# Kernel tuning notes

Measured on AMD Instinct MI355X. Metric: run time of the kernel, lower is better.

Reference implementation:

```python
import jax, jax.numpy as jnp
import numpy as np

N = 50000
E = 400000
IN_DIM = 16
EMB = 32
HID = 128
HEADS = 4
LAYERS = 3
EPS_BN = 1e-5
NEG_SLOPE = 0.2


def setup_inputs() -> dict:
    key = jax.random.key(0)
    ks = jax.random.split(key, 16)
    s = 0.1
    C = HID  # per-head out channels (concat=False)
    inp = {
        "x": jax.random.normal(ks[0], (N, IN_DIM), jnp.float32),
        "edge_index": jax.random.randint(ks[1], (2, E), 0, N, jnp.int64),
        "emb": s * jax.random.normal(ks[2], (N, EMB), jnp.float32),
        "Wf": s * jax.random.normal(ks[3], (EMB, IN_DIM), jnp.float32),
        "bf": jnp.zeros((EMB,), jnp.float32),
        "Wc": s * jax.random.normal(ks[4], (HID, 2 * EMB), jnp.float32),
        "bc": jnp.zeros((HID,), jnp.float32),
        "Wl": s * jax.random.normal(ks[5], (LAYERS, HEADS * C, HID), jnp.float32),
        "a_src": s * jax.random.normal(ks[6], (LAYERS, HEADS, C), jnp.float32),
        "a_dst": s * jax.random.normal(ks[7], (LAYERS, HEADS, C), jnp.float32),
        "bl": jnp.zeros((LAYERS, C), jnp.float32),
        "gamma": jnp.ones((LAYERS, C), jnp.float32),
        "beta": jnp.zeros((LAYERS, C), jnp.float32),
        "Wout": s * jax.random.normal(ks[8], (1, HID), jnp.float32),
        "bout": jnp.zeros((1,), jnp.float32),
    }
    return inp


def _gat_layer(h, src, dst, W, a_s, a_d, b):
    n = h.shape[0]
    C = W.shape[0] // HEADS
    hp = (h @ W.T).reshape(n, HEADS, C)                # (N,H,C)
    al_s = jnp.sum(hp * a_s, axis=-1)                  # (N,H)
    al_d = jnp.sum(hp * a_d, axis=-1)                  # (N,H)
    e = jax.nn.leaky_relu(al_s[src] + al_d[dst], NEG_SLOPE)  # (E,H)
    m = jax.ops.segment_max(e, dst, num_segments=n)    # per-target max
    ex = jnp.exp(e - m[dst])
    denom = jax.ops.segment_sum(ex, dst, num_segments=n) + 1e-16
    alpha = ex / denom[dst]                            # (E,H)
    msg = hp[src] * alpha[..., None]                   # (E,H,C)
    out = jax.ops.segment_sum(msg, dst, num_segments=n)
    return jnp.mean(out, axis=1) + b                   # concat=False: head mean


def _bn(x, g, b):
    mu = jnp.mean(x, axis=0)
    var = jnp.var(x, axis=0)  # biased, as torch BN uses for normalization
    return (x - mu) * jax.lax.rsqrt(var + EPS_BN) * g + b


def reference(x, edge_index, emb, Wf, bf, Wc, bc, Wl, a_src, a_dst, bl, gamma, beta, Wout, bout):
    n = x.shape[0]
    loop = jnp.arange(n, dtype=edge_index.dtype)
    src = jnp.concatenate([edge_index[0], loop])       # add self loops
    dst = jnp.concatenate([edge_index[1], loop])
    feat = x @ Wf.T + bf
    h = jax.nn.relu(jnp.concatenate([emb, feat], axis=1) @ Wc.T + bc)
    prev_h = h
    for i in range(LAYERS):
        h = _gat_layer(h, src, dst, Wl[i], a_src[i], a_dst[i], bl[i])
        h = jax.nn.relu(_bn(h, gamma[i], beta[i]))
        if prev_h.shape == h.shape:
            h = h + prev_h
        prev_h = h
    out = h @ Wout.T + bout
    return jnp.clip(out, -10.0, 10.0)
```

## Files before the change

kernel.cpp:

```cpp
#include <hip/hip_runtime.h>
#include <hip/hip_bf16.h>
#include <math.h>

#define INDIM 16
#define EMBD 32
#define UDIM 64
#define HIDD 128
#define HEADS 4
#define LAYERS 3
#define MPAD 50048

typedef short v8s __attribute__((ext_vector_type(8)));
typedef float v4f __attribute__((ext_vector_type(4)));

__device__ __forceinline__ float lrelu(float x) { return x > 0.f ? x : 0.2f * x; }
__device__ __forceinline__ float bf2f(unsigned int bits16) {
    unsigned int u = bits16 << 16;
    return __builtin_bit_cast(float, u);
}
__device__ __forceinline__ unsigned short f2bf(float f) {
    unsigned int u = __builtin_bit_cast(unsigned int, f);
    unsigned int lsb = (u >> 16) & 1;
    u += 0x7fff + lsb;
    return (unsigned short)(u >> 16);
}

__global__ __launch_bounds__(256) void k_enc(const float* __restrict__ x,
                                             const float* __restrict__ emb,
                                             const float* __restrict__ Wf,
                                             const float* __restrict__ bf,
                                             unsigned short* __restrict__ u, int n) {
    int i = blockIdx.x * 256 + threadIdx.x;
    if (i >= n * EMBD) return;
    int node = i >> 5, j = i & 31;
    const float* xr = x + (size_t)node * INDIM;
    const float* wr = Wf + (size_t)j * INDIM;
    float s = bf[j];
#pragma unroll
    for (int k = 0; k < INDIM; k++) s += xr[k] * wr[k];
    u[(size_t)node * UDIM + EMBD + j] = f2bf(s);
    u[(size_t)node * UDIM + j] = f2bf(emb[(size_t)node * EMBD + j]);
}

__global__ __launch_bounds__(256) void k_prep_v(const float* __restrict__ Wl,
                                                unsigned short* __restrict__ Vb) {
    int i = blockIdx.x * 256 + threadIdx.x;
    if (i >= LAYERS * HIDD * 512) return;
    int l = i >> 16;
    int rem = i & 65535;
    int c = rem >> 9;
    int f = rem & 511;
    int h = f >> 7, k = f & 127;
    Vb[i] = f2bf(Wl[(size_t)l * 512 * HIDD + (size_t)(h * HIDD + c) * HIDD + k]);
}

__global__ __launch_bounds__(256) void k_prep_a(const float* __restrict__ Wl,
                                                const float* __restrict__ a_s,
                                                const float* __restrict__ a_d,
                                                float* __restrict__ ws, float* __restrict__ wd) {
    int i = blockIdx.x * 256 + threadIdx.x;
    if (i >= LAYERS * HEADS * HIDD) return;
    int l = i >> 9, h = (i >> 7) & 3, k = i & 127;
    const float* W = Wl + (size_t)l * 512 * HIDD;
    const float* as = a_s + l * 512 + h * HIDD;
    const float* ad = a_d + l * 512 + h * HIDD;
    float ss = 0.f, sd = 0.f;
    for (int c = 0; c < HIDD; c++) {
        float w = W[(size_t)(h * HIDD + c) * HIDD + k];
        ss += as[c] * w;
        sd += ad[c] * w;
    }
    ws[i] = ss;
    wd[i] = sd;
}

__global__ __launch_bounds__(256) void k_prep_wc(const float* __restrict__ Wc,
                                                 unsigned short* __restrict__ Wcb) {
    int i = blockIdx.x * 256 + threadIdx.x;
    if (i < HIDD * UDIM) Wcb[i] = f2bf(Wc[i]);
}

__global__ __launch_bounds__(256) void k_gemm_enc(const unsigned short* __restrict__ A,
                                                  const unsigned short* __restrict__ B,
                                                  const float* __restrict__ bias,
                                                  float* __restrict__ O,
                                                  unsigned short* __restrict__ Ob, int M) {
    const int K = UDIM;
    int tid = threadIdx.x;
    int lane = tid & 63, wid = tid >> 6;
    int wm = wid >> 1, wn = wid & 1;
    int bm = blockIdx.x * 128;
    int lr = lane & 15, lk = lane >> 4;
    v4f acc[4][4] = {};
    const unsigned short* Abase = A + (size_t)(bm + wm * 64 + lr) * K + lk * 8;
    const unsigned short* Bbase = B + (size_t)(wn * 64 + lr) * K + lk * 8;
#pragma unroll
    for (int kk = 0; kk < K / 32; kk++) {
        v8s a[4], b[4];
#pragma unroll
        for (int f = 0; f < 4; f++) {
            a[f] = *(const v8s*)(Abase + (size_t)(f * 16) * K + kk * 32);
            b[f] = *(const v8s*)(Bbase + (size_t)(f * 16) * K + kk * 32);
        }
#pragma unroll
        for (int i = 0; i < 4; i++)
#pragma unroll
            for (int j = 0; j < 4; j++)
                acc[i][j] = __builtin_amdgcn_mfma_f32_16x16x32_bf16(a[i], b[j], acc[i][j], 0, 0, 0);
    }
#pragma unroll
    for (int i = 0; i < 4; i++) {
#pragma unroll
        for (int r = 0; r < 4; r++) {
            int row = bm + wm * 64 + i * 16 + lk * 4 + r;
            if (row >= M) continue;
#pragma unroll
            for (int j = 0; j < 4; j++) {
                int col = wn * 64 + j * 16 + lr;
                float v = fmaxf(acc[i][j][r] + bias[col], 0.f);
                O[(size_t)row * HIDD + col] = v;
                Ob[(size_t)row * HIDD + col] = f2bf(v);
            }
        }
    }
}

__global__ __launch_bounds__(256) void k_deg(const int* __restrict__ ei, int* __restrict__ deg,
                                             int E, int tot) {
    int e = blockIdx.x * 256 + threadIdx.x;
    if (e >= tot) return;
    int dst = (e < E) ? ei[E + e] : (e - E);
    atomicAdd(&deg[dst], 1);
}

__global__ __launch_bounds__(256) void k_scan1(const int* __restrict__ deg,
                                               int* __restrict__ rowptr,
                                               int* __restrict__ partials, int n) {
    int tid = threadIdx.x;
    int i = blockIdx.x * 256 + tid;
    int v = (i < n) ? deg[i] : 0;
    __shared__ int sm[256];
    sm[tid] = v;
    __syncthreads();
    for (int off = 1; off < 256; off <<= 1) {
        int t = (tid >= off) ? sm[tid - off] : 0;
        __syncthreads();
        sm[tid] += t;
        __syncthreads();
    }
    if (i < n) rowptr[i] = sm[tid] - v;
    if (tid == 255) partials[blockIdx.x] = sm[255];
}

__global__ __launch_bounds__(256) void k_scan2(int* __restrict__ partials, int nb) {
    int tid = threadIdx.x;
    int v = (tid < nb) ? partials[tid] : 0;
    __shared__ int sm[256];
    sm[tid] = v;
    __syncthreads();
    for (int off = 1; off < 256; off <<= 1) {
        int t = (tid >= off) ? sm[tid - off] : 0;
        __syncthreads();
        sm[tid] += t;
        __syncthreads();
    }
    if (tid < nb) partials[tid] = sm[tid] - v;
}

__global__ __launch_bounds__(256) void k_scan3(const int* __restrict__ deg,
                                               const int* __restrict__ partials,
                                               int* __restrict__ rowptr,
                                               int* __restrict__ cursor, int n) {
    int i = blockIdx.x * 256 + threadIdx.x;
    if (i >= n) return;
    int r = rowptr[i] + partials[blockIdx.x];
    rowptr[i] = r;
    cursor[i] = r;
    if (i == n - 1) rowptr[n] = r + deg[i];
}

__global__ __launch_bounds__(256) void k_scatter(const int* __restrict__ ei, int* __restrict__ cursor,
                                                 int* __restrict__ csr_src, int E, int tot) {
    int e = blockIdx.x * 256 + threadIdx.x;
    if (e >= tot) return;
    int src = (e < E) ? ei[e] : (e - E);
    int dst = (e < E) ? ei[E + e] : (e - E);
    int pos = atomicAdd(&cursor[dst], 1);
    csr_src[pos] = src;
}

__global__ __launch_bounds__(256) void k_al0(const float* __restrict__ h,
                                             const float* __restrict__ ws,
                                             const float* __restrict__ wd,
                                             float* __restrict__ al_s, float* __restrict__ al_d,
                                             int n) {
    int wid = threadIdx.x >> 6, lane = threadIdx.x & 63;
    int node = blockIdx.x * 4 + wid;
    if (node >= n) return;
    float2 v = *(const float2*)(h + (size_t)node * HIDD + 2 * lane);
    float s[8];
#pragma unroll
    for (int hh = 0; hh < 4; hh++) {
        float2 w1 = *(const float2*)(ws + hh * HIDD + 2 * lane);
        float2 w2 = *(const float2*)(wd + hh * HIDD + 2 * lane);
        s[hh] = v.x * w1.x + v.y * w1.y;
        s[4 + hh] = v.x * w2.x + v.y * w2.y;
    }
#pragma unroll
    for (int o = 32; o; o >>= 1)
#pragma unroll
        for (int q = 0; q < 8; q++) s[q] += __shfl_xor(s[q], o);
    if (lane == 0) {
        *(float4*)(al_s + (size_t)node * 4) = make_float4(s[0], s[1], s[2], s[3]);
        *(float4*)(al_d + (size_t)node * 4) = make_float4(s[4], s[5], s[6], s[7]);
    }
}

__global__ __launch_bounds__(1024) void k_layer(const int* __restrict__ rowptr,
                                                const int* __restrict__ csr_src,
                                                const float* __restrict__ al_s,
                                                const float* __restrict__ al_d,
                                                const unsigned short* __restrict__ hb,
                                                const unsigned short* __restrict__ Vb,
                                                float* __restrict__ agg,
                                                float* __restrict__ bns, int n) {
    __shared__ unsigned int Gw[16 * 256];
    __shared__ float s1[128], s2[128];
    int tid = threadIdx.x, lane = tid & 63, w = tid >> 6;
    if (tid < 128) { s1[tid] = 0.f; s2[tid] = 0.f; }
    int node0 = blockIdx.x * 16;
    int node = node0 + w;
    const float4* als4 = (const float4*)al_s;
    const unsigned int* h2 = (const unsigned int*)hb;
    float acc[4][2] = {};

    if (node < n) {
        int start = rowptr[node], end = rowptr[node + 1];
        int deg = end - start;
        float4 ad = ((const float4*)al_d)[node];
        if (deg <= 64) {
            bool act = lane < deg;
            int src_l = act ? csr_src[start + lane] : 0;
            float e0 = -3.0e38f, e1 = -3.0e38f, e2 = -3.0e38f, e3 = -3.0e38f;
            if (act) {
                float4 as = als4[src_l];
                e0 = lrelu(as.x + ad.x);
                e1 = lrelu(as.y + ad.y);
                e2 = lrelu(as.z + ad.z);
                e3 = lrelu(as.w + ad.w);
            }
            float m0 = e0, m1 = e1, m2 = e2, m3 = e3;
#pragma unroll
            for (int o = 32; o; o >>= 1) {
                m0 = fmaxf(m0, __shfl_xor(m0, o));
                m1 = fmaxf(m1, __shfl_xor(m1, o));
                m2 = fmaxf(m2, __shfl_xor(m2, o));
                m3 = fmaxf(m3, __shfl_xor(m3, o));
            }
            float p0 = act ? expf(e0 - m0) : 0.f;
            float p1 = act ? expf(e1 - m1) : 0.f;
            float p2 = act ? expf(e2 - m2) : 0.f;
            float p3 = act ? expf(e3 - m3) : 0.f;
            float t0 = p0, t1 = p1, t2 = p2, t3 = p3;
#pragma unroll
            for (int o = 32; o; o >>= 1) {
                t0 += __shfl_xor(t0, o);
                t1 += __shfl_xor(t1, o);
                t2 += __shfl_xor(t2, o);
                t3 += __shfl_xor(t3, o);
            }
            float a0 = p0 / (t0 + 1e-16f), a1 = p1 / (t1 + 1e-16f);
            float a2 = p2 / (t2 + 1e-16f), a3 = p3 / (t3 + 1e-16f);
            int jj = 0;
            for (; jj + 2 <= deg; jj += 2) {
                int sj0 = __shfl(src_l, jj), sj1 = __shfl(src_l, jj + 1);
                unsigned int u0 = h2[(size_t)sj0 * 64 + lane];
                unsigned int u1 = h2[(size_t)sj1 * 64 + lane];
                float b00 = __shfl(a0, jj), b01 = __shfl(a1, jj);
                float b02 = __shfl(a2, jj), b03 = __shfl(a3, jj);
                float b10 = __shfl(a0, jj + 1), b11 = __shfl(a1, jj + 1);
                float b12 = __shfl(a2, jj + 1), b13 = __shfl(a3, jj + 1);
                float x00 = bf2f(u0 & 0xffff), x01 = bf2f(u0 >> 16);
                float x10 = bf2f(u1 & 0xffff), x11 = bf2f(u1 >> 16);
                acc[0][0] += b00 * x00 + b10 * x10; acc[0][1] += b00 * x01 + b10 * x11;
                acc[1][0] += b01 * x00 + b11 * x10; acc[1][1] += b01 * x01 + b11 * x11;
                acc[2][0] += b02 * x00 + b12 * x10; acc[2][1] += b02 * x01 + b12 * x11;
                acc[3][0] += b03 * x00 + b13 * x10; acc[3][1] += b03 * x01 + b13 * x11;
            }
            if (jj < deg) {
                int sj = __shfl(src_l, jj);
                unsigned int uu = h2[(size_t)sj * 64 + lane];
                float b0 = __shfl(a0, jj), b1 = __shfl(a1, jj);
                float b2 = __shfl(a2, jj), b3 = __shfl(a3, jj);
                float x0 = bf2f(uu & 0xffff), x1 = bf2f(uu >> 16);
                acc[0][0] += b0 * x0; acc[0][1] += b0 * x1;
                acc[1][0] += b1 * x0; acc[1][1] += b1 * x1;
                acc[2][0] += b2 * x0; acc[2][1] += b2 * x1;
                acc[3][0] += b3 * x0; acc[3][1] += b3 * x1;
            }
        } else {
            float m0 = -3.0e38f, m1 = -3.0e38f, m2 = -3.0e38f, m3 = -3.0e38f;
            for (int j = start + lane; j < end; j += 64) {
                float4 as = als4[csr_src[j]];
                m0 = fmaxf(m0, lrelu(as.x + ad.x));
                m1 = fmaxf(m1, lrelu(as.y + ad.y));
                m2 = fmaxf(m2, lrelu(as.z + ad.z));
                m3 = fmaxf(m3, lrelu(as.w + ad.w));
            }
#pragma unroll
            for (int o = 32; o; o >>= 1) {
                m0 = fmaxf(m0, __shfl_xor(m0, o));
                m1 = fmaxf(m1, __shfl_xor(m1, o));
                m2 = fmaxf(m2, __shfl_xor(m2, o));
                m3 = fmaxf(m3, __shfl_xor(m3, o));
            }
            float t0 = 0.f, t1 = 0.f, t2 = 0.f, t3 = 0.f;
            for (int j = start + lane; j < end; j += 64) {
                float4 as = als4[csr_src[j]];
                t0 += expf(lrelu(as.x + ad.x) - m0);
                t1 += expf(lrelu(as.y + ad.y) - m1);
                t2 += expf(lrelu(as.z + ad.z) - m2);
                t3 += expf(lrelu(as.w + ad.w) - m3);
            }
#pragma unroll
            for (int o = 32; o; o >>= 1) {
                t0 += __shfl_xor(t0, o);
                t1 += __shfl_xor(t1, o);
                t2 += __shfl_xor(t2, o);
                t3 += __shfl_xor(t3, o);
            }
            float i0 = 1.f / (t0 + 1e-16f), i1 = 1.f / (t1 + 1e-16f);
            float i2 = 1.f / (t2 + 1e-16f), i3 = 1.f / (t3 + 1e-16f);
            for (int base = start; base < end; base += 64) {
                int cnt = min(64, end - base);
                bool act = lane < cnt;
                int src_l = act ? csr_src[base + lane] : 0;
                float a0 = 0.f, a1 = 0.f, a2 = 0.f, a3 = 0.f;
                if (act) {
                    float4 as = als4[src_l];
                    a0 = expf(lrelu(as.x + ad.x) - m0) * i0;
                    a1 = expf(lrelu(as.y + ad.y) - m1) * i1;
                    a2 = expf(lrelu(as.z + ad.z) - m2) * i2;
                    a3 = expf(lrelu(as.w + ad.w) - m3) * i3;
                }
                for (int jj = 0; jj < cnt; jj++) {
                    int sj = __shfl(src_l, jj);
                    float b0 = __shfl(a0, jj), b1 = __shfl(a1, jj);
                    float b2 = __shfl(a2, jj), b3 = __shfl(a3, jj);
                    unsigned int uu = h2[(size_t)sj * 64 + lane];
                    float x0 = bf2f(uu & 0xffff), x1 = bf2f(uu >> 16);
                    acc[0][0] += b0 * x0; acc[0][1] += b0 * x1;
                    acc[1][0] += b1 * x0; acc[1][1] += b1 * x1;
                    acc[2][0] += b2 * x0; acc[2][1] += b2 * x1;
                    acc[3][0] += b3 * x0; acc[3][1] += b3 * x1;
                }
            }
        }
    }
    {
        int sw = (w & 7) << 2;
#pragma unroll
        for (int hh = 0; hh < 4; hh++) {
            unsigned int p = (unsigned int)f2bf(acc[hh][0]) | ((unsigned int)f2bf(acc[hh][1]) << 16);
            Gw[w * 256 + ((hh * 64 + lane) ^ sw)] = p;
        }
    }
    __syncthreads();

    if (w < 8) {
        int lr = lane & 15, lk = lane >> 4;
        int swr = (lr & 7) << 2;
        v4f a2 = {};
        const unsigned short* Bb = Vb + (size_t)(w * 16 + lr) * 512 + lk * 8;
#pragma unroll
        for (int kk = 0; kk < 16; kk++) {
            v8s a = *(const v8s*)(&Gw[lr * 256 + ((kk * 16 + lk * 4) ^ swr)]);
            v8s b = *(const v8s*)(Bb + kk * 32);
            a2 = __builtin_amdgcn_mfma_f32_16x16x32_bf16(a, b, a2, 0, 0, 0);
        }
        int col = w * 16 + lr;
        float ls = 0.f, lq = 0.f;
#pragma unroll
        for (int r = 0; r < 4; r++) {
            int nd = node0 + lk * 4 + r;
            float v = a2[r];
            if (nd < n) {
                agg[(size_t)nd * HIDD + col] = v;
                ls += v;
                lq += v * v;
            }
        }
        atomicAdd(&s1[col], ls);
        atomicAdd(&s2[col], lq);
    }
    __syncthreads();
    if (tid < 128) {
        atomicAdd(&bns[tid], s1[tid]);
        atomicAdd(&bns[128 + tid], s2[tid]);
    }
}

template <int MODE>
__global__ __launch_bounds__(256) void k_apply(const float* __restrict__ agg,
                                               const float* __restrict__ bns,
                                               const float* __restrict__ gamma,
                                               const float* __restrict__ beta,
                                               float* __restrict__ h,
                                               unsigned short* __restrict__ hb,
                                               const float* __restrict__ ws,
                                               const float* __restrict__ wd,
                                               float* __restrict__ al_s,
                                               float* __restrict__ al_d,
                                               const float* __restrict__ Wout,
                                               const float* __restrict__ bout,
                                               float* __restrict__ out,
                                               float invn, int n) {
    int wid = threadIdx.x >> 6, lane = threadIdx.x & 63;
    int node = blockIdx.x * 4 + wid;
    if (node >= n) return;
    int c0 = 2 * lane, c1 = 2 * lane + 1;
    float2 ag = *(const float2*)(agg + (size_t)node * HIDD + c0);
    float2 ho = *(const float2*)(h + (size_t)node * HIDD + c0);
    float mu0 = bns[c0] * invn, mu1 = bns[c1] * invn;
    float va0 = bns[128 + c0] * invn - mu0 * mu0;
    float va1 = bns[128 + c1] * invn - mu1 * mu1;
    float sc0 = gamma[c0] * rsqrtf(0.0625f * va0 + 1e-5f);
    float sc1 = gamma[c1] * rsqrtf(0.0625f * va1 + 1e-5f);
    float v0 = fmaxf((ag.x - mu0) * 0.25f * sc0 + beta[c0], 0.f) + ho.x;
    float v1 = fmaxf((ag.y - mu1) * 0.25f * sc1 + beta[c1], 0.f) + ho.y;
    if (MODE == 0) {
        *(float2*)(h + (size_t)node * HIDD + c0) = make_float2(v0, v1);
        ((unsigned int*)hb)[(size_t)node * 64 + lane] =
            (unsigned int)f2bf(v0) | ((unsigned int)f2bf(v1) << 16);
        float s[8];
#pragma unroll
        for (int hh = 0; hh < 4; hh++) {
            float2 w1 = *(const float2*)(ws + hh * HIDD + c0);
            float2 w2 = *(const float2*)(wd + hh * HIDD + c0);
            s[hh] = v0 * w1.x + v1 * w1.y;
            s[4 + hh] = v0 * w2.x + v1 * w2.y;
        }
#pragma unroll
        for (int o = 32; o; o >>= 1)
#pragma unroll
            for (int q = 0; q < 8; q++) s[q] += __shfl_xor(s[q], o);
        if (lane == 0) {
            *(float4*)(al_s + (size_t)node * 4) = make_float4(s[0], s[1], s[2], s[3]);
            *(float4*)(al_d + (size_t)node * 4) = make_float4(s[4], s[5], s[6], s[7]);
        }
    } else {
        float2 w = *(const float2*)(Wout + c0);
        float p = v0 * w.x + v1 * w.y;
#pragma unroll
        for (int o = 32; o; o >>= 1) p += __shfl_xor(p, o);
        if (lane == 0) {
            float v = p + bout[0];
            out[node] = fminf(fmaxf(v, -10.f), 10.f);
        }
    }
}

extern "C" void kernel_launch(void* const* d_in, const int* in_sizes, int n_in,
                              void* d_out, int out_size, void* d_ws, size_t ws_size,
                              hipStream_t stream) {
    const float* x = (const float*)d_in[0];
    const int* ei = (const int*)d_in[1];
    const float* emb = (const float*)d_in[2];
    const float* Wf = (const float*)d_in[3];
    const float* bf = (const float*)d_in[4];
    const float* Wc = (const float*)d_in[5];
    const float* bc = (const float*)d_in[6];
    const float* Wl = (const float*)d_in[7];
    const float* a_src = (const float*)d_in[8];
    const float* a_dst = (const float*)d_in[9];
    const float* gamma = (const float*)d_in[11];
    const float* beta = (const float*)d_in[12];
    const float* Wout = (const float*)d_in[13];
    const float* bout = (const float*)d_in[14];
    float* out = (float*)d_out;

    int n = in_sizes[0] / INDIM;
    int E = in_sizes[1] / 2;
    int tot = E + n;
    int NB = (n + 255) / 256;

    size_t off = 0;
    auto alloc = [&](size_t bytes) {
        void* p = (char*)d_ws + off;
        off = (off + bytes + 255) & ~(size_t)255;
        return p;
    };
    unsigned short* u = (unsigned short*)alloc((size_t)MPAD * UDIM * 2);
    float* h = (float*)alloc((size_t)MPAD * HIDD * 4);
    unsigned short* hb = (unsigned short*)alloc((size_t)MPAD * HIDD * 2);
    float* agg = (float*)alloc((size_t)MPAD * HIDD * 4);
    float* al_s = (float*)alloc((size_t)n * HEADS * 4);
    float* al_d = (float*)alloc((size_t)n * HEADS * 4);
    int* deg = (int*)alloc((size_t)n * 4);
    int* rowptr = (int*)alloc(((size_t)n + 1) * 4);
    int* cursor = (int*)alloc((size_t)n * 4);
    int* csr_src = (int*)alloc((size_t)tot * 4);
    int* partials = (int*)alloc((size_t)NB * 4);
    unsigned short* Vb = (unsigned short*)alloc((size_t)LAYERS * HIDD * 512 * 2);
    unsigned short* Wcb = (unsigned short*)alloc((size_t)HIDD * UDIM * 2);
    float* ws = (float*)alloc((size_t)LAYERS * HEADS * HIDD * 4);
    float* wd = (float*)alloc((size_t)LAYERS * HEADS * HIDD * 4);
    float* bnsums = (float*)alloc(LAYERS * 256 * 4);
    (void)ws_size;

    hipMemsetAsync(deg, 0, (size_t)n * 4, stream);
    hipMemsetAsync(bnsums, 0, LAYERS * 256 * 4, stream);
    if (n < MPAD) {
        hipMemsetAsync(u + (size_t)n * UDIM, 0, (size_t)(MPAD - n) * UDIM * 2, stream);
    }

    k_prep_v<<<(LAYERS * HIDD * 512 + 255) / 256, 256, 0, stream>>>(Wl, Vb);
    k_prep_a<<<(LAYERS * HEADS * HIDD + 255) / 256, 256, 0, stream>>>(Wl, a_src, a_dst, ws, wd);
    k_prep_wc<<<(HIDD * UDIM + 255) / 256, 256, 0, stream>>>(Wc, Wcb);

    k_deg<<<(tot + 255) / 256, 256, 0, stream>>>(ei, deg, E, tot);
    k_scan1<<<NB, 256, 0, stream>>>(deg, rowptr, partials, n);
    k_scan2<<<1, 256, 0, stream>>>(partials, NB);
    k_scan3<<<NB, 256, 0, stream>>>(deg, partials, rowptr, cursor, n);
    k_scatter<<<(tot + 255) / 256, 256, 0, stream>>>(ei, cursor, csr_src, E, tot);

    k_enc<<<(n * EMBD + 255) / 256, 256, 0, stream>>>(x, emb, Wf, bf, u, n);
    k_gemm_enc<<<MPAD / 128, 256, 0, stream>>>(u, Wcb, bc, h, hb, n);
    k_al0<<<(n + 3) / 4, 256, 0, stream>>>(h, ws, wd, al_s, al_d, n);

    float invn = 1.0f / (float)n;
    int NLB = (n + 15) / 16;
    for (int l = 0; l < LAYERS; l++) {
        k_layer<<<NLB, 1024, 0, stream>>>(rowptr, csr_src, al_s, al_d, hb,
                                          Vb + (size_t)l * HIDD * 512, agg,
                                          bnsums + l * 256, n);
        if (l < LAYERS - 1)
            k_apply<0><<<(n + 3) / 4, 256, 0, stream>>>(
                agg, bnsums + l * 256, gamma + l * HIDD, beta + l * HIDD, h, hb,
                ws + (size_t)(l + 1) * 512, wd + (size_t)(l + 1) * 512, al_s, al_d,
                nullptr, nullptr, nullptr, invn, n);
        else
            k_apply<1><<<(n + 3) / 4, 256, 0, stream>>>(
                agg, bnsums + l * 256, gamma + l * HIDD, beta + l * HIDD, h, hb,
                nullptr, nullptr, nullptr, nullptr, Wout, bout, out, invn, n);
    }
}
```

Baseline: 512.0 us.

## Sort nodes by in-degree so each layer block processes similar-degree nodes

```diff
diff --git a/kernel.cpp b/kernel.cpp
--- a/kernel.cpp
+++ b/kernel.cpp
@@ -189,6 +189,36 @@
     csr_src[pos] = src;
 }
 
+__global__ __launch_bounds__(256) void k_hist(const int* __restrict__ deg, int* __restrict__ hist,
+                                              int n) {
+    int i = blockIdx.x * 256 + threadIdx.x;
+    if (i < n) atomicAdd(&hist[min(deg[i], 255)], 1);
+}
+
+__global__ __launch_bounds__(256) void k_hscan(int* __restrict__ hist) {
+    int tid = threadIdx.x;
+    int v = hist[tid];
+    __shared__ int sm[256];
+    sm[tid] = v;
+    __syncthreads();
+    for (int off = 1; off < 256; off <<= 1) {
+        int t = (tid >= off) ? sm[tid - off] : 0;
+        __syncthreads();
+        sm[tid] += t;
+        __syncthreads();
+    }
+    hist[tid] = sm[tid] - v;
+}
+
+__global__ __launch_bounds__(256) void k_psort(const int* __restrict__ deg, int* __restrict__ hist,
+                                               int* __restrict__ perm, int n) {
+    int i = blockIdx.x * 256 + threadIdx.x;
+    if (i >= n) return;
+    int b = min(deg[i], 255);
+    int p = atomicAdd(&hist[b], 1);
+    perm[p] = i;
+}
+
 __global__ __launch_bounds__(256) void k_al0(const float* __restrict__ h,
                                              const float* __restrict__ ws,
                                              const float* __restrict__ wd,
@@ -218,6 +248,7 @@
 
 __global__ __launch_bounds__(1024) void k_layer(const int* __restrict__ rowptr,
                                                 const int* __restrict__ csr_src,
+                                                const int* __restrict__ perm,
                                                 const float* __restrict__ al_s,
                                                 const float* __restrict__ al_d,
                                                 const unsigned short* __restrict__ hb,
@@ -226,15 +257,18 @@
                                                 float* __restrict__ bns, int n) {
     __shared__ unsigned int Gw[16 * 256];
     __shared__ float s1[128], s2[128];
+    __shared__ int pnode[16];
     int tid = threadIdx.x, lane = tid & 63, w = tid >> 6;
     if (tid < 128) { s1[tid] = 0.f; s2[tid] = 0.f; }
     int node0 = blockIdx.x * 16;
-    int node = node0 + w;
+    int idx = node0 + w;
+    int node = (idx < n) ? perm[idx] : -1;
+    if (lane == 0) pnode[w] = node;
     const float4* als4 = (const float4*)al_s;
     const unsigned int* h2 = (const unsigned int*)hb;
     float acc[4][2] = {};
 
-    if (node < n) {
+    if (node >= 0) {
         int start = rowptr[node], end = rowptr[node + 1];
         int deg = end - start;
         float4 ad = ((const float4*)al_d)[node];
@@ -249,9 +283,10 @@
                 e2 = lrelu(as.z + ad.z);
                 e3 = lrelu(as.w + ad.w);
             }
+            int span = 1;
+            while (span < deg) span <<= 1;
             float m0 = e0, m1 = e1, m2 = e2, m3 = e3;
-#pragma unroll
-            for (int o = 32; o; o >>= 1) {
+            for (int o = 1; o < span; o <<= 1) {
                 m0 = fmaxf(m0, __shfl_xor(m0, o));
                 m1 = fmaxf(m1, __shfl_xor(m1, o));
                 m2 = fmaxf(m2, __shfl_xor(m2, o));
@@ -262,8 +297,7 @@
             float p2 = act ? expf(e2 - m2) : 0.f;
             float p3 = act ? expf(e3 - m3) : 0.f;
             float t0 = p0, t1 = p1, t2 = p2, t3 = p3;
-#pragma unroll
-            for (int o = 32; o; o >>= 1) {
+            for (int o = 1; o < span; o <<= 1) {
                 t0 += __shfl_xor(t0, o);
                 t1 += __shfl_xor(t1, o);
                 t2 += __shfl_xor(t2, o);
@@ -382,9 +416,9 @@
         float ls = 0.f, lq = 0.f;
 #pragma unroll
         for (int r = 0; r < 4; r++) {
-            int nd = node0 + lk * 4 + r;
+            int nd = pnode[lk * 4 + r];
             float v = a2[r];
-            if (nd < n) {
+            if (nd >= 0) {
                 agg[(size_t)nd * HIDD + col] = v;
                 ls += v;
                 lq += v * v;
@@ -501,6 +535,8 @@
     int* cursor = (int*)alloc((size_t)n * 4);
     int* csr_src = (int*)alloc((size_t)tot * 4);
     int* partials = (int*)alloc((size_t)NB * 4);
+    int* hist = (int*)alloc(256 * 4);
+    int* perm = (int*)alloc((size_t)n * 4);
     unsigned short* Vb = (unsigned short*)alloc((size_t)LAYERS * HIDD * 512 * 2);
     unsigned short* Wcb = (unsigned short*)alloc((size_t)HIDD * UDIM * 2);
     float* ws = (float*)alloc((size_t)LAYERS * HEADS * HIDD * 4);
@@ -509,6 +545,7 @@
     (void)ws_size;
 
     hipMemsetAsync(deg, 0, (size_t)n * 4, stream);
+    hipMemsetAsync(hist, 0, 256 * 4, stream);
     hipMemsetAsync(bnsums, 0, LAYERS * 256 * 4, stream);
     if (n < MPAD) {
         hipMemsetAsync(u + (size_t)n * UDIM, 0, (size_t)(MPAD - n) * UDIM * 2, stream);
@@ -523,6 +560,9 @@
     k_scan2<<<1, 256, 0, stream>>>(partials, NB);
     k_scan3<<<NB, 256, 0, stream>>>(deg, partials, rowptr, cursor, n);
     k_scatter<<<(tot + 255) / 256, 256, 0, stream>>>(ei, cursor, csr_src, E, tot);
+    k_hist<<<NB, 256, 0, stream>>>(deg, hist, n);
+    k_hscan<<<1, 256, 0, stream>>>(hist);
+    k_psort<<<NB, 256, 0, stream>>>(deg, hist, perm, n);
 
     k_enc<<<(n * EMBD + 255) / 256, 256, 0, stream>>>(x, emb, Wf, bf, u, n);
     k_gemm_enc<<<MPAD / 128, 256, 0, stream>>>(u, Wcb, bc, h, hb, n);
@@ -531,7 +571,7 @@
     float invn = 1.0f / (float)n;
     int NLB = (n + 15) / 16;
     for (int l = 0; l < LAYERS; l++) {
-        k_layer<<<NLB, 1024, 0, stream>>>(rowptr, csr_src, al_s, al_d, hb,
+        k_layer<<<NLB, 1024, 0, stream>>>(rowptr, csr_src, perm, al_s, al_d, hb,
                                           Vb + (size_t)l * HIDD * 512, agg,
                                           bnsums + l * 256, n);
         if (l < LAYERS - 1)
```

After: 855.5 us. 67.1% more time.

## Split low-degree GAT aggregation across 4 edge groups, slice BN atomics

Applied to the files above, without the earlier changes.

```diff
diff --git a/kernel.cpp b/kernel.cpp
--- a/kernel.cpp
+++ b/kernel.cpp
@@ -9,6 +9,7 @@
 #define HEADS 4
 #define LAYERS 3
 #define MPAD 50048
+#define NSLICE 32
 
 typedef short v8s __attribute__((ext_vector_type(8)));
 typedef float v4f __attribute__((ext_vector_type(4)));
@@ -232,7 +233,7 @@
     int node = node0 + w;
     const float4* als4 = (const float4*)al_s;
     const unsigned int* h2 = (const unsigned int*)hb;
-    float acc[4][2] = {};
+    int sw = (w & 7) << 2;
 
     if (node < n) {
         int start = rowptr[node], end = rowptr[node + 1];
@@ -249,9 +250,10 @@
                 e2 = lrelu(as.z + ad.z);
                 e3 = lrelu(as.w + ad.w);
             }
+            int span = 1;
+            while (span < deg) span <<= 1;
             float m0 = e0, m1 = e1, m2 = e2, m3 = e3;
-#pragma unroll
-            for (int o = 32; o; o >>= 1) {
+            for (int o = 1; o < span; o <<= 1) {
                 m0 = fmaxf(m0, __shfl_xor(m0, o));
                 m1 = fmaxf(m1, __shfl_xor(m1, o));
                 m2 = fmaxf(m2, __shfl_xor(m2, o));
@@ -262,8 +264,7 @@
             float p2 = act ? expf(e2 - m2) : 0.f;
             float p3 = act ? expf(e3 - m3) : 0.f;
             float t0 = p0, t1 = p1, t2 = p2, t3 = p3;
-#pragma unroll
-            for (int o = 32; o; o >>= 1) {
+            for (int o = 1; o < span; o <<= 1) {
                 t0 += __shfl_xor(t0, o);
                 t1 += __shfl_xor(t1, o);
                 t2 += __shfl_xor(t2, o);
@@ -271,33 +272,51 @@
             }
             float a0 = p0 / (t0 + 1e-16f), a1 = p1 / (t1 + 1e-16f);
             float a2 = p2 / (t2 + 1e-16f), a3 = p3 / (t3 + 1e-16f);
-            int jj = 0;
-            for (; jj + 2 <= deg; jj += 2) {
-                int sj0 = __shfl(src_l, jj), sj1 = __shfl(src_l, jj + 1);
-                unsigned int u0 = h2[(size_t)sj0 * 64 + lane];
-                unsigned int u1 = h2[(size_t)sj1 * 64 + lane];
-                float b00 = __shfl(a0, jj), b01 = __shfl(a1, jj);
-                float b02 = __shfl(a2, jj), b03 = __shfl(a3, jj);
-                float b10 = __shfl(a0, jj + 1), b11 = __shfl(a1, jj + 1);
-                float b12 = __shfl(a2, jj + 1), b13 = __shfl(a3, jj + 1);
-                float x00 = bf2f(u0 & 0xffff), x01 = bf2f(u0 >> 16);
-                float x10 = bf2f(u1 & 0xffff), x11 = bf2f(u1 >> 16);
-                acc[0][0] += b00 * x00 + b10 * x10; acc[0][1] += b00 * x01 + b10 * x11;
-                acc[1][0] += b01 * x00 + b11 * x10; acc[1][1] += b01 * x01 + b11 * x11;
-                acc[2][0] += b02 * x00 + b12 * x10; acc[2][1] += b02 * x01 + b12 * x11;
-                acc[3][0] += b03 * x00 + b13 * x10; acc[3][1] += b03 * x01 + b13 * x11;
-            }
-            if (jj < deg) {
-                int sj = __shfl(src_l, jj);
-                unsigned int uu = h2[(size_t)sj * 64 + lane];
-                float b0 = __shfl(a0, jj), b1 = __shfl(a1, jj);
-                float b2 = __shfl(a2, jj), b3 = __shfl(a3, jj);
-                float x0 = bf2f(uu & 0xffff), x1 = bf2f(uu >> 16);
-                acc[0][0] += b0 * x0; acc[0][1] += b0 * x1;
-                acc[1][0] += b1 * x0; acc[1][1] += b1 * x1;
-                acc[2][0] += b2 * x0; acc[2][1] += b2 * x1;
-                acc[3][0] += b3 * x0; acc[3][1] += b3 * x1;
-            }
+
+            int el = lane >> 4, cg = lane & 15;
+            float acc[4][8] = {};
+            int nch = (deg + 3) >> 2;
+            for (int c = 0; c < nch; c += 2) {
+                int j0 = c * 4 + el;
+                int j1 = j0 + 4;
+                int s0 = __shfl(src_l, j0);
+                int s1v = __shfl(src_l, j1);
+                float b00 = __shfl(a0, j0), b01 = __shfl(a1, j0);
+                float b02 = __shfl(a2, j0), b03 = __shfl(a3, j0);
+                float b10 = __shfl(a0, j1), b11 = __shfl(a1, j1);
+                float b12 = __shfl(a2, j1), b13 = __shfl(a3, j1);
+                uint4 u0 = *(const uint4*)(h2 + (size_t)s0 * 64 + cg * 4);
+                uint4 u1 = *(const uint4*)(h2 + (size_t)s1v * 64 + cg * 4);
+#pragma unroll
+                for (int q = 0; q < 4; q++) {
+                    unsigned int w0 = ((const unsigned int*)&u0)[q];
+                    unsigned int w1 = ((const unsigned int*)&u1)[q];
+                    float x00 = bf2f(w0 & 0xffff), x01 = bf2f(w0 >> 16);
+                    float x10 = bf2f(w1 & 0xffff), x11 = bf2f(w1 >> 16);
+                    acc[0][2 * q] += b00 * x00 + b10 * x10;
+                    acc[0][2 * q + 1] += b00 * x01 + b10 * x11;
+                    acc[1][2 * q] += b01 * x00 + b11 * x10;
+                    acc[1][2 * q + 1] += b01 * x01 + b11 * x11;
+                    acc[2][2 * q] += b02 * x00 + b12 * x10;
+                    acc[2][2 * q + 1] += b02 * x01 + b12 * x11;
+                    acc[3][2 * q] += b03 * x00 + b13 * x10;
+                    acc[3][2 * q + 1] += b03 * x01 + b13 * x11;
+                }
+            }
+#pragma unroll
+            for (int hh = 0; hh < 4; hh++)
+#pragma unroll
+                for (int q = 0; q < 8; q++) {
+                    acc[hh][q] += __shfl_xor(acc[hh][q], 16);
+                    acc[hh][q] += __shfl_xor(acc[hh][q], 32);
+                }
+            unsigned int pk[4];
+#pragma unroll
+            for (int q = 0; q < 4; q++)
+                pk[q] = (unsigned int)f2bf(acc[el][2 * q]) |
+                        ((unsigned int)f2bf(acc[el][2 * q + 1]) << 16);
+            int base = el * 64 + cg * 4;
+            *(uint4*)&Gw[w * 256 + (base ^ sw)] = *(uint4*)pk;
         } else {
             float m0 = -3.0e38f, m1 = -3.0e38f, m2 = -3.0e38f, m3 = -3.0e38f;
             for (int j = start + lane; j < end; j += 64) {
@@ -331,6 +350,7 @@
             }
             float i0 = 1.f / (t0 + 1e-16f), i1 = 1.f / (t1 + 1e-16f);
             float i2 = 1.f / (t2 + 1e-16f), i3 = 1.f / (t3 + 1e-16f);
+            float acc[4][2] = {};
             for (int base = start; base < end; base += 64) {
                 int cnt = min(64, end - base);
                 bool act = lane < cnt;
@@ -355,15 +375,18 @@
                     acc[3][0] += b3 * x0; acc[3][1] += b3 * x1;
                 }
             }
-        }
-    }
-    {
-        int sw = (w & 7) << 2;
-#pragma unroll
-        for (int hh = 0; hh < 4; hh++) {
-            unsigned int p = (unsigned int)f2bf(acc[hh][0]) | ((unsigned int)f2bf(acc[hh][1]) << 16);
-            Gw[w * 256 + ((hh * 64 + lane) ^ sw)] = p;
-        }
+#pragma unroll
+            for (int hh = 0; hh < 4; hh++) {
+                unsigned int p = (unsigned int)f2bf(acc[hh][0]) |
+                                 ((unsigned int)f2bf(acc[hh][1]) << 16);
+                Gw[w * 256 + ((hh * 64 + lane) ^ sw)] = p;
+            }
+        }
+    } else {
+        int el = lane >> 4, cg = lane & 15;
+        int base = el * 64 + cg * 4;
+        uint4 z = {0, 0, 0, 0};
+        *(uint4*)&Gw[w * 256 + (base ^ sw)] = z;
     }
     __syncthreads();
 
@@ -395,16 +418,34 @@
     }
     __syncthreads();
     if (tid < 128) {
-        atomicAdd(&bns[tid], s1[tid]);
-        atomicAdd(&bns[128 + tid], s2[tid]);
-    }
+        float* slice = bns + (size_t)(blockIdx.x & (NSLICE - 1)) * 256;
+        atomicAdd(&slice[tid], s1[tid]);
+        atomicAdd(&slice[128 + tid], s2[tid]);
+    }
+}
+
+__global__ __launch_bounds__(128) void k_bnfin(const float* __restrict__ bns,
+                                               const float* __restrict__ gamma,
+                                               const float* __restrict__ beta,
+                                               float* __restrict__ scale,
+                                               float* __restrict__ shift, float invn) {
+    int c = threadIdx.x;
+    float s = 0.f, q = 0.f;
+    for (int sl = 0; sl < NSLICE; sl++) {
+        s += bns[sl * 256 + c];
+        q += bns[sl * 256 + 128 + c];
+    }
+    float mu = s * invn;
+    float var = q * invn - mu * mu;
+    float sc = gamma[c] * rsqrtf(0.0625f * var + 1e-5f) * 0.25f;
+    scale[c] = sc;
+    shift[c] = beta[c] - mu * sc;
 }
 
 template <int MODE>
 __global__ __launch_bounds__(256) void k_apply(const float* __restrict__ agg,
-                                               const float* __restrict__ bns,
-                                               const float* __restrict__ gamma,
-                                               const float* __restrict__ beta,
+                                               const float* __restrict__ scale,
+                                               const float* __restrict__ shift,
                                                float* __restrict__ h,
                                                unsigned short* __restrict__ hb,
                                                const float* __restrict__ ws,
@@ -413,21 +454,15 @@
                                                float* __restrict__ al_d,
                                                const float* __restrict__ Wout,
                                                const float* __restrict__ bout,
-                                               float* __restrict__ out,
-                                               float invn, int n) {
+                                               float* __restrict__ out, int n) {
     int wid = threadIdx.x >> 6, lane = threadIdx.x & 63;
     int node = blockIdx.x * 4 + wid;
     if (node >= n) return;
     int c0 = 2 * lane, c1 = 2 * lane + 1;
     float2 ag = *(const float2*)(agg + (size_t)node * HIDD + c0);
     float2 ho = *(const float2*)(h + (size_t)node * HIDD + c0);
-    float mu0 = bns[c0] * invn, mu1 = bns[c1] * invn;
-    float va0 = bns[128 + c0] * invn - mu0 * mu0;
-    float va1 = bns[128 + c1] * invn - mu1 * mu1;
-    float sc0 = gamma[c0] * rsqrtf(0.0625f * va0 + 1e-5f);
-    float sc1 = gamma[c1] * rsqrtf(0.0625f * va1 + 1e-5f);
-    float v0 = fmaxf((ag.x - mu0) * 0.25f * sc0 + beta[c0], 0.f) + ho.x;
-    float v1 = fmaxf((ag.y - mu1) * 0.25f * sc1 + beta[c1], 0.f) + ho.y;
+    float v0 = fmaxf(ag.x * scale[c0] + shift[c0], 0.f) + ho.x;
+    float v1 = fmaxf(ag.y * scale[c1] + shift[c1], 0.f) + ho.y;
     if (MODE == 0) {
         *(float2*)(h + (size_t)node * HIDD + c0) = make_float2(v0, v1);
         ((unsigned int*)hb)[(size_t)node * 64 + lane] =
@@ -505,11 +540,13 @@
     unsigned short* Wcb = (unsigned short*)alloc((size_t)HIDD * UDIM * 2);
     float* ws = (float*)alloc((size_t)LAYERS * HEADS * HIDD * 4);
     float* wd = (float*)alloc((size_t)LAYERS * HEADS * HIDD * 4);
-    float* bnsums = (float*)alloc(LAYERS * 256 * 4);
+    float* bnsums = (float*)alloc((size_t)LAYERS * NSLICE * 256 * 4);
+    float* scale = (float*)alloc(128 * 4);
+    float* shift = (float*)alloc(128 * 4);
     (void)ws_size;
 
     hipMemsetAsync(deg, 0, (size_t)n * 4, stream);
-    hipMemsetAsync(bnsums, 0, LAYERS * 256 * 4, stream);
+    hipMemsetAsync(bnsums, 0, (size_t)LAYERS * NSLICE * 256 * 4, stream);
     if (n < MPAD) {
         hipMemsetAsync(u + (size_t)n * UDIM, 0, (size_t)(MPAD - n) * UDIM * 2, stream);
     }
@@ -533,15 +570,17 @@
     for (int l = 0; l < LAYERS; l++) {
         k_layer<<<NLB, 1024, 0, stream>>>(rowptr, csr_src, al_s, al_d, hb,
                                           Vb + (size_t)l * HIDD * 512, agg,
-                                          bnsums + l * 256, n);
+                                          bnsums + (size_t)l * NSLICE * 256, n);
+        k_bnfin<<<1, 128, 0, stream>>>(bnsums + (size_t)l * NSLICE * 256, gamma + l * HIDD,
+                                       beta + l * HIDD, scale, shift, invn);
         if (l < LAYERS - 1)
             k_apply<0><<<(n + 3) / 4, 256, 0, stream>>>(
-                agg, bnsums + l * 256, gamma + l * HIDD, beta + l * HIDD, h, hb,
+                agg, scale, shift, h, hb,
                 ws + (size_t)(l + 1) * 512, wd + (size_t)(l + 1) * 512, al_s, al_d,
-                nullptr, nullptr, nullptr, invn, n);
+                nullptr, nullptr, nullptr, n);
         else
             k_apply<1><<<(n + 3) / 4, 256, 0, stream>>>(
-                agg, bnsums + l * 256, gamma + l * HIDD, beta + l * HIDD, h, hb,
-                nullptr, nullptr, nullptr, nullptr, Wout, bout, out, invn, n);
-    }
-}
+                agg, scale, shift, h, hb,
+                nullptr, nullptr, nullptr, nullptr, Wout, bout, out, n);
+    }
+}
```

New measurement: 748.9 us. +46.3%, slower.
